# Kernel tuning notes

Measured on AMD Instinct MI355X. Metric: run time of the kernel, lower is better.

## Reference

```python
import jax, jax.numpy as jnp
import numpy as np

N = 50000       # nodes
E = 800000      # edges (avg degree 16)
IN = 256        # input feature dim
HID = 64        # per-head hidden dim
H = 2           # heads
C = 64          # num_classes (final single-head layer width)
NEG_SLOPE = 0.01  # torch F.leaky_relu default


def setup_inputs() -> dict:
    key = jax.random.key(0)
    ks = jax.random.split(key, 24)
    nrm = lambda k, shape, scale: jax.random.normal(k, shape, jnp.float32) * scale
    features = nrm(ks[0], (N, IN), 1.0)
    src = jax.random.randint(ks[1], (E,), 0, N)
    dst = jax.random.randint(ks[2], (E,), 0, N)
    # layer 0: H heads, Linear(IN->HID) + attn_l/attn_r Linear(HID->1)
    W0 = nrm(ks[3], (H, IN, HID), IN ** -0.5)
    b0 = jnp.zeros((H, HID), jnp.float32)
    al0 = nrm(ks[4], (H, HID), HID ** -0.5)
    bl0 = jnp.zeros((H,), jnp.float32)
    ar0 = nrm(ks[5], (H, HID), HID ** -0.5)
    br0 = jnp.zeros((H,), jnp.float32)
    # layer 1: H heads, Linear(H*HID->HID)
    W1 = nrm(ks[6], (H, H * HID, HID), (H * HID) ** -0.5)
    b1 = jnp.zeros((H, HID), jnp.float32)
    al1 = nrm(ks[7], (H, HID), HID ** -0.5)
    bl1 = jnp.zeros((H,), jnp.float32)
    ar1 = nrm(ks[8], (H, HID), HID ** -0.5)
    br1 = jnp.zeros((H,), jnp.float32)
    # final: 1 head, Linear(H*HID->C)
    Wf = nrm(ks[9], (1, H * HID, C), (H * HID) ** -0.5)
    bf = jnp.zeros((1, C), jnp.float32)
    alf = nrm(ks[10], (1, C), C ** -0.5)
    blf = jnp.zeros((1,), jnp.float32)
    arf = nrm(ks[11], (1, C), C ** -0.5)
    brf = jnp.zeros((1,), jnp.float32)
    return dict(features=features, src=src, dst=dst,
                W0=W0, b0=b0, al0=al0, bl0=bl0, ar0=ar0, br0=br0,
                W1=W1, b1=b1, al1=al1, bl1=bl1, ar1=ar1, br1=br1,
                Wf=Wf, bf=bf, alf=alf, blf=blf, arf=arf, brf=brf)


def gat_layer(x, src, dst, W, b, al, bl, ar, br):
    # x: [N, D]; W: [H, D, K]
    ft = jnp.einsum('nd,hdk->nhk', x, W) + b          # [N,H,K]
    a1 = jnp.einsum('nhk,hk->nh', ft, al) + bl        # [N,H] (dst-side)
    a2 = jnp.einsum('nhk,hk->nh', ft, ar) + br        # [N,H] (src-side)
    s = jax.nn.leaky_relu(a1[dst] + a2[src], NEG_SLOPE)  # [E,H]
    m = jax.ops.segment_max(s, dst, num_segments=N)      # per-dst max for stable softmax
    e = jnp.exp(s - m[dst])
    denom = jax.ops.segment_sum(e, dst, num_segments=N)
    alpha = e / denom[dst]                               # edge softmax over in-neighbors
    accum = jax.ops.segment_sum(alpha[:, :, None] * ft[src], dst, num_segments=N)  # [N,H,K]
    return jax.nn.elu(accum)


def reference(features, src, dst,
              W0, b0, al0, bl0, ar0, br0,
              W1, b1, al1, bl1, ar1, br1,
              Wf, bf, alf, blf, arf, brf):
    x = gat_layer(features, src, dst, W0, b0, al0, bl0, ar0, br0).reshape(N, H * HID)
    x = gat_layer(x, src, dst, W1, b1, al1, bl1, ar1, br1).reshape(N, H * HID)
    out = gat_layer(x, src, dst, Wf, bf, alf, blf, arf, brf)[:, 0, :]  # [N,C]
    return out
```

## Files before the change

kernel.cpp:

```cpp
#include <hip/hip_runtime.h>
#include <math.h>

#define NN 50000
#define EE 800000
#define DIN 256
#define NEG_SLOPE 0.01f

typedef __attribute__((ext_vector_type(8))) short bf16x8;
typedef __attribute__((ext_vector_type(8))) unsigned short u16x8;
typedef __attribute__((ext_vector_type(4))) float f32x4;
typedef __attribute__((ext_vector_type(2))) _Float16 f16x2;

__device__ __forceinline__ unsigned short bf16_rne(float f) {
    unsigned int u = __float_as_uint(f);
    u += 0x7fffu + ((u >> 16) & 1u);
    return (unsigned short)(u >> 16);
}
__device__ __forceinline__ float bf16_tof(unsigned short h) {
    return __uint_as_float(((unsigned int)h) << 16);
}

__device__ __forceinline__ void fmamix_lo(float& a, unsigned f, float w) {
    asm("v_fma_mix_f32 %0, %1, %2, %0 op_sel:[0,0,0] op_sel_hi:[1,0,0]"
        : "+v"(a)
        : "v"(f), "v"(w));
}
__device__ __forceinline__ void fmamix_hi(float& a, unsigned f, float w) {
    asm("v_fma_mix_f32 %0, %1, %2, %0 op_sel:[1,0,0] op_sel_hi:[1,0,0]"
        : "+v"(a)
        : "v"(f), "v"(w));
}

__global__ __launch_bounds__(1024) void scanA_kernel(const int* __restrict__ cnt,
                                                     int* __restrict__ off,
                                                     int* __restrict__ aux, int Nn) {
    __shared__ int wsums[16];
    int tid = threadIdx.x, lane = tid & 63, w = tid >> 6;
    int i = blockIdx.x * 1024 + tid;
    int v = (i < Nn) ? cnt[i] : 0;
    int x = v;
#pragma unroll
    for (int d = 1; d < 64; d <<= 1) {
        int y = __shfl_up(x, d);
        if (lane >= d) x += y;
    }
    if (lane == 63) wsums[w] = x;
    __syncthreads();
    if (w == 0 && lane < 16) {
        int ws = wsums[lane];
#pragma unroll
        for (int d = 1; d < 16; d <<= 1) {
            int y = __shfl_up(ws, d);
            if (lane >= d) ws += y;
        }
        wsums[lane] = ws;
    }
    __syncthreads();
    int incl = x + (w > 0 ? wsums[w - 1] : 0);
    if (i < Nn) off[i + 1] = incl;
    if (tid == 1023) aux[blockIdx.x] = incl;
}

__global__ __launch_bounds__(1024) void scanC_kernel(const int* __restrict__ aux,
                                                     int* __restrict__ off, int Nn) {
    int b = blockIdx.x;
    int prefix = 0;
    for (int j = 0; j < b; j++) prefix += aux[j];
    int i = b * 1024 + threadIdx.x;
    if (i < Nn) off[i + 1] += prefix;
    if (i == 0 && b == 0) off[0] = 0;
}

__global__ __launch_bounds__(256) void scatter_kernel(const int* __restrict__ src,
                                                      const int* __restrict__ dst,
                                                      const int* __restrict__ off,
                                                      const int* __restrict__ pos,
                                                      int* __restrict__ esrc, int E) {
    int e = blockIdx.x * 256 + threadIdx.x;
    if (e >= E) return;
    int d = dst[e];
    esrc[off[d] + pos[e]] = src[e];
}

__global__ __launch_bounds__(256) void conv_w_kernel(
    const float* __restrict__ W0, const float* __restrict__ W1,
    const float* __restrict__ Wf, unsigned short* __restrict__ w0h,
    unsigned short* __restrict__ w0l, unsigned short* __restrict__ w1h,
    unsigned short* __restrict__ w1l, unsigned short* __restrict__ wfh,
    unsigned short* __restrict__ wfl) {
    int t = blockIdx.x * 256 + threadIdx.x;
    const float* W;
    unsigned short *oh, *ol;
    int D, u;
    if (t < 32768) { W = W0; oh = w0h; ol = w0l; D = 256; u = t; }
    else if (t < 49152) { W = W1; oh = w1h; ol = w1l; D = 128; u = t - 32768; }
    else if (t < 57344) { W = Wf; oh = wfh; ol = wfl; D = 128; u = t - 49152; }
    else return;
    int d = u & (D - 1);
    int n = u / D;
    float v = W[((size_t)(n >> 6) * D + d) * 64 + (n & 63)];
    unsigned short hi = bf16_rne(v);
    unsigned short lo = bf16_rne(v - bf16_tof(hi));
    oh[(size_t)n * D + d] = hi;
    ol[(size_t)n * D + d] = lo;
}

#define LDK 40

template <int NCOL, bool AFP32, bool HIST>
__global__ __launch_bounds__(256) void gemm_attn(
    const float* __restrict__ Xf, const unsigned short* __restrict__ Xhi,
    const unsigned short* __restrict__ Xlo, const unsigned short* __restrict__ Wthi,
    const unsigned short* __restrict__ Wtlo, const float* __restrict__ bias,
    const float* __restrict__ al, const float* __restrict__ bl,
    const float* __restrict__ ar, const float* __restrict__ br,
    _Float16* __restrict__ FT, float* __restrict__ A1, float* __restrict__ A2,
    int Nn, int D, const int* __restrict__ edst, int* __restrict__ cnt,
    int* __restrict__ pos, int E, int gemmBlocks) {
    if (HIST) {
        if ((int)blockIdx.x >= gemmBlocks) {
            int e = ((int)blockIdx.x - gemmBlocks) * 256 + threadIdx.x;
            if (e < E) pos[e] = atomicAdd(&cnt[edst[e]], 1);
            return;
        }
    }
    const int H = NCOL / 64;
    const int NC16 = NCOL / 16;
    __shared__ __align__(16) unsigned short Ahi_s[64 * LDK];
    __shared__ __align__(16) unsigned short Alo_s[64 * LDK];
    __shared__ __align__(16) unsigned short Bhi_s[NCOL * LDK];
    __shared__ __align__(16) unsigned short Blo_s[NCOL * LDK];

    int tid = threadIdx.x;
    int wv = tid >> 6, l = tid & 63, lm = l & 15, quad = l >> 4;
    int m0 = blockIdx.x * 64;

    f32x4 acc[NC16];
#pragma unroll
    for (int c = 0; c < NC16; c++) acc[c] = (f32x4){0.f, 0.f, 0.f, 0.f};

    for (int d0 = 0; d0 < D; d0 += 32) {
        if (AFP32) {
#pragma unroll
            for (int i = 0; i < 2; i++) {
                int u = tid + i * 256;
                int row = u >> 3, c4 = u & 7;
                float4 v = make_float4(0.f, 0.f, 0.f, 0.f);
                if (m0 + row < Nn)
                    v = *(const float4*)&Xf[(size_t)(m0 + row) * D + d0 + c4 * 4];
                float f[4] = {v.x, v.y, v.z, v.w};
                unsigned short hi[4], lo[4];
#pragma unroll
                for (int j = 0; j < 4; j++) {
                    hi[j] = bf16_rne(f[j]);
                    lo[j] = bf16_rne(f[j] - bf16_tof(hi[j]));
                }
                *(ushort4*)&Ahi_s[row * LDK + c4 * 4] = make_ushort4(hi[0], hi[1], hi[2], hi[3]);
                *(ushort4*)&Alo_s[row * LDK + c4 * 4] = make_ushort4(lo[0], lo[1], lo[2], lo[3]);
            }
        } else {
            int row = tid >> 2, q = tid & 3;
            u16x8 vh = (u16x8)0, vl = (u16x8)0;
            if (m0 + row < Nn) {
                vh = *(const u16x8*)&Xhi[(size_t)(m0 + row) * D + d0 + q * 8];
                vl = *(const u16x8*)&Xlo[(size_t)(m0 + row) * D + d0 + q * 8];
            }
            *(u16x8*)&Ahi_s[row * LDK + q * 8] = vh;
            *(u16x8*)&Alo_s[row * LDK + q * 8] = vl;
        }
#pragma unroll
        for (int i = 0; i < NCOL / 64; i++) {
            int u = tid + i * 256;
            int n = u >> 2, q = u & 3;
            *(u16x8*)&Bhi_s[n * LDK + q * 8] =
                *(const u16x8*)&Wthi[(size_t)n * D + d0 + q * 8];
            *(u16x8*)&Blo_s[n * LDK + q * 8] =
                *(const u16x8*)&Wtlo[(size_t)n * D + d0 + q * 8];
        }
        __syncthreads();

        int arow = wv * 16 + lm;
        bf16x8 ah = *(const bf16x8*)&Ahi_s[arow * LDK + quad * 8];
        bf16x8 alo = *(const bf16x8*)&Alo_s[arow * LDK + quad * 8];
#pragma unroll
        for (int cg = 0; cg < NC16; cg += 4) {
            bf16x8 bh4[4], bl4[4];
#pragma unroll
            for (int u = 0; u < 4; u++) {
                bh4[u] = *(const bf16x8*)&Bhi_s[((cg + u) * 16 + lm) * LDK + quad * 8];
                bl4[u] = *(const bf16x8*)&Blo_s[((cg + u) * 16 + lm) * LDK + quad * 8];
            }
#pragma unroll
            for (int u = 0; u < 4; u++)
                acc[cg + u] = __builtin_amdgcn_mfma_f32_16x16x32_bf16(ah, bh4[u], acc[cg + u], 0, 0, 0);
#pragma unroll
            for (int u = 0; u < 4; u++)
                acc[cg + u] = __builtin_amdgcn_mfma_f32_16x16x32_bf16(ah, bl4[u], acc[cg + u], 0, 0, 0);
#pragma unroll
            for (int u = 0; u < 4; u++)
                acc[cg + u] = __builtin_amdgcn_mfma_f32_16x16x32_bf16(alo, bh4[u], acc[cg + u], 0, 0, 0);
        }
        __syncthreads();
    }

    float bj[NC16], alj[NC16], arj[NC16];
#pragma unroll
    for (int c = 0; c < NC16; c++) {
        bj[c] = bias[c * 16 + lm];
        alj[c] = al[c * 16 + lm];
        arj[c] = ar[c * 16 + lm];
    }
#pragma unroll
    for (int reg = 0; reg < 4; reg++) {
        int row = m0 + wv * 16 + quad * 4 + reg;
        bool ok = row < Nn;
        float s1[H], s2[H];
#pragma unroll
        for (int h = 0; h < H; h++) { s1[h] = 0.f; s2[h] = 0.f; }
#pragma unroll
        for (int c = 0; c < NC16; c++) {
            float o = acc[c][reg] + bj[c];
            int h = c >> 2;
            s1[h] += o * alj[c];
            s2[h] += o * arj[c];
            if (ok) FT[(size_t)row * NCOL + c * 16 + lm] = (_Float16)o;
        }
#pragma unroll
        for (int h = 0; h < H; h++) {
#pragma unroll
            for (int d = 1; d < 16; d <<= 1) {
                s1[h] += __shfl_xor(s1[h], d);
                s2[h] += __shfl_xor(s2[h], d);
            }
        }
        if (ok && lm == 0) {
#pragma unroll
            for (int h = 0; h < H; h++) {
                A1[(size_t)row * H + h] = s1[h] + bl[h];
                A2[(size_t)row * H + h] = s2[h] + br[h];
            }
        }
    }
}

__global__ __launch_bounds__(256) void agg2_kernel(
    const _Float16* __restrict__ ft, const float* __restrict__ a1,
    const float* __restrict__ a2, const int* __restrict__ off,
    const int* __restrict__ esrc, unsigned short* __restrict__ ohi,
    unsigned short* __restrict__ olo, int Nn) {
    __shared__ __align__(16) int2 pk0s[4][64];
    __shared__ __align__(16) int2 pk1s[4][64];
    int wv = threadIdx.x >> 6, lane = threadIdx.x & 63;
    int n = blockIdx.x * 4 + wv;
    if (n >= Nn) return;
    int o0 = off[n], deg = off[n + 1] - o0;
    int hs = lane >> 5, cl2 = lane * 2;
    unsigned lb = (unsigned)lane * 4u;
    if (deg == 0) {
        *(ushort2*)&ohi[(size_t)n * 128 + cl2] = make_ushort2(0, 0);
        *(ushort2*)&olo[(size_t)n * 128 + cl2] = make_ushort2(0, 0);
        return;
    }
    const char* ftb = (const char*)ft;
    const int2* pw = hs ? pk1s[wv] : pk0s[wv];
    float2 a1v = *(const float2*)&a1[(size_t)n * 2];
    float ax = 0.f, ay = 0.f;
    float ds0 = 0.f, ds1 = 0.f;
    for (int e0 = 0; e0 < deg; e0 += 64) {
        int nE = min(64, deg - e0);
        float w0 = 0.f, w1 = 0.f;
        int sj = 0;
        if (lane < nE) {
            sj = esrc[o0 + e0 + lane];
            float2 a2j = *(const float2*)((const char*)a2 + ((unsigned)sj << 3));
            float t0 = a1v.x + a2j.x;
            float t1 = a1v.y + a2j.y;
            t0 = t0 > 0.f ? t0 : NEG_SLOPE * t0;
            t1 = t1 > 0.f ? t1 : NEG_SLOPE * t1;
            w0 = __expf(t0);
            w1 = __expf(t1);
        }
        ds0 += w0;
        ds1 += w1;
        pk0s[wv][lane] = make_int2(sj, __float_as_int(w0));
        pk1s[wv][lane] = make_int2(sj, __float_as_int(w1));
        int nB = (nE + 15) >> 4;
        for (int b = 0; b < nB; b++) {
            int j = b * 16;
            int2 pb[16];
#pragma unroll
            for (int u = 0; u < 16; u++) pb[u] = pw[j + u];
            unsigned f[16];
#pragma unroll
            for (int u = 0; u < 16; u++)
                f[u] = *(const unsigned*)(ftb + (((unsigned)pb[u].x << 8) + lb));
#pragma unroll
            for (int u = 0; u < 16; u++) {
                float w = __int_as_float(pb[u].y);
                fmamix_lo(ax, f[u], w);
                fmamix_hi(ay, f[u], w);
            }
        }
    }
#pragma unroll
    for (int d = 1; d < 64; d <<= 1) {
        ds0 += __shfl_xor(ds0, d);
        ds1 += __shfl_xor(ds1, d);
    }
    float rd = 1.f / (hs ? ds1 : ds0);
    float rx = ax * rd, ry = ay * rd;
    rx = rx > 0.f ? rx : expm1f(rx);
    ry = ry > 0.f ? ry : expm1f(ry);
    unsigned short hx = bf16_rne(rx), hy = bf16_rne(ry);
    unsigned short lx = bf16_rne(rx - bf16_tof(hx)), ly = bf16_rne(ry - bf16_tof(hy));
    *(ushort2*)&ohi[(size_t)n * 128 + cl2] = make_ushort2(hx, hy);
    *(ushort2*)&olo[(size_t)n * 128 + cl2] = make_ushort2(lx, ly);
}

__global__ __launch_bounds__(256) void agg1_kernel(
    const _Float16* __restrict__ ft, const float* __restrict__ a1,
    const float* __restrict__ a2, const int* __restrict__ off,
    const int* __restrict__ esrc, float* __restrict__ out, int Nn) {
    __shared__ __align__(16) int2 pks[4][64];
    int wv = threadIdx.x >> 6, lane = threadIdx.x & 63;
    int n = blockIdx.x * 4 + wv;
    if (n >= Nn) return;
    int o0 = off[n], deg = off[n + 1] - o0;
    if (deg == 0) {
        out[(size_t)n * 64 + lane] = 0.f;
        return;
    }
    const char* ftb = (const char*)ft;
    unsigned lb = (unsigned)lane * 2u;
    float a1v = a1[n];
    float acc = 0.f, dsum = 0.f;
    for (int e0 = 0; e0 < deg; e0 += 64) {
        int nE = min(64, deg - e0);
        float wl = 0.f;
        int sj = 0;
        if (lane < nE) {
            sj = esrc[o0 + e0 + lane];
            float t = a1v + a2[sj];
            t = t > 0.f ? t : NEG_SLOPE * t;
            wl = __expf(t);
        }
        dsum += wl;
        pks[wv][lane] = make_int2(sj, __float_as_int(wl));
        int nB = (nE + 15) >> 4;
        for (int b = 0; b < nB; b++) {
            int j = b * 16;
            int2 pb[16];
#pragma unroll
            for (int u = 0; u < 16; u++) pb[u] = pks[wv][j + u];
            unsigned f[16];
#pragma unroll
            for (int u = 0; u < 16; u++)
                f[u] = *(const unsigned short*)(ftb + (((unsigned)pb[u].x << 7) + lb));
#pragma unroll
            for (int u = 0; u < 16; u++)
                fmamix_lo(acc, f[u], __int_as_float(pb[u].y));
        }
    }
#pragma unroll
    for (int d = 1; d < 64; d <<= 1) dsum += __shfl_xor(dsum, d);
    float r = acc / dsum;
    out[(size_t)n * 64 + lane] = r > 0.f ? r : expm1f(r);
}

extern "C" void kernel_launch(void* const* d_in, const int* in_sizes, int n_in,
                              void* d_out, int out_size, void* d_ws, size_t ws_size,
                              hipStream_t stream) {
    const float* features = (const float*)d_in[0];
    const int* src = (const int*)d_in[1];
    const int* dst = (const int*)d_in[2];
    const float* W0 = (const float*)d_in[3];
    const float* b0 = (const float*)d_in[4];
    const float* al0 = (const float*)d_in[5];
    const float* bl0 = (const float*)d_in[6];
    const float* ar0 = (const float*)d_in[7];
    const float* br0 = (const float*)d_in[8];
    const float* W1 = (const float*)d_in[9];
    const float* b1 = (const float*)d_in[10];
    const float* al1 = (const float*)d_in[11];
    const float* bl1 = (const float*)d_in[12];
    const float* ar1 = (const float*)d_in[13];
    const float* br1 = (const float*)d_in[14];
    const float* Wf = (const float*)d_in[15];
    const float* bf = (const float*)d_in[16];
    const float* alf = (const float*)d_in[17];
    const float* blf = (const float*)d_in[18];
    const float* arf = (const float*)d_in[19];
    const float* brf = (const float*)d_in[20];

    char* p = (char*)d_ws;
    auto carve = [&](size_t bytes) {
        void* q = (void*)p;
        p += (bytes + 255) & ~(size_t)255;
        return q;
    };
    _Float16* ft = (_Float16*)carve((size_t)NN * 128 * 2);
    unsigned short* Xhi = (unsigned short*)carve((size_t)NN * 128 * 2);
    unsigned short* Xlo = (unsigned short*)carve((size_t)NN * 128 * 2);
    float* a1 = (float*)carve((size_t)NN * 2 * 4);
    float* a2 = (float*)carve((size_t)NN * 2 * 4);
    int* off = (int*)carve((size_t)(NN + 1) * 4);
    int* cnt = (int*)carve((size_t)NN * 4);
    int* esrc = (int*)carve((size_t)EE * 4);
    int* pos = (int*)carve((size_t)EE * 4);
    int* aux = (int*)carve(64 * 4);
    unsigned short* w0h = (unsigned short*)carve(32768 * 2);
    unsigned short* w0l = (unsigned short*)carve(32768 * 2);
    unsigned short* w1h = (unsigned short*)carve(16384 * 2);
    unsigned short* w1l = (unsigned short*)carve(16384 * 2);
    unsigned short* wfh = (unsigned short*)carve(8192 * 2);
    unsigned short* wfl = (unsigned short*)carve(8192 * 2);

    const int NB_SCAN = (NN + 1023) / 1024;
    const int GE = (EE + 255) / 256;

    const int gx = (NN + 63) / 64;
    const int gn = (NN + 3) / 4;

    hipMemsetAsync(cnt, 0, (size_t)NN * 4, stream);
    conv_w_kernel<<<(57344 + 255) / 256, 256, 0, stream>>>(W0, W1, Wf, w0h, w0l, w1h,
                                                           w1l, wfh, wfl);

    gemm_attn<128, true, true><<<gx + GE, 256, 0, stream>>>(
        features, nullptr, nullptr, w0h, w0l, b0, al0, bl0, ar0, br0, ft, a1, a2,
        NN, DIN, dst, cnt, pos, EE, gx);

    scanA_kernel<<<NB_SCAN, 1024, 0, stream>>>(cnt, off, aux, NN);
    scanC_kernel<<<NB_SCAN, 1024, 0, stream>>>(aux, off, NN);
    scatter_kernel<<<GE, 256, 0, stream>>>(src, dst, off, pos, esrc, EE);

    agg2_kernel<<<gn, 256, 0, stream>>>(ft, a1, a2, off, esrc, Xhi, Xlo, NN);

    gemm_attn<128, false, false><<<gx, 256, 0, stream>>>(
        nullptr, Xhi, Xlo, w1h, w1l, b1, al1, bl1, ar1, br1, ft, a1, a2, NN, 128,
        nullptr, nullptr, nullptr, 0, 0);
    agg2_kernel<<<gn, 256, 0, stream>>>(ft, a1, a2, off, esrc, Xhi, Xlo, NN);

    gemm_attn<64, false, false><<<gx, 256, 0, stream>>>(
        nullptr, Xhi, Xlo, wfh, wfl, bf, alf, blf, arf, brf, ft, a1, a2, NN, 128,
        nullptr, nullptr, nullptr, 0, 0);
    agg1_kernel<<<gn, 256, 0, stream>>>(ft, a1, a2, off, esrc, (float*)d_out, NN);
}
```

Before: 301.6 us.

## Double GEMM row tile to 128 so each wave reuses B fragments across two row groups

The fused GEMM+attention kernel now computes 128 rows per block instead of 64. Each wave handles two 16-row groups with separate accumulators, so every B-fragment load from shared memory feeds twice as many MFMAs and the weight tile is staged half as often overall. The cost is double the accumulator registers and a larger LDS footprint, which may lower occupancy. The grid also halves, to about 391 GEMM blocks, which cuts parallelism on a many-CU GPU.

```diff
diff --git a/kernel.cpp b/kernel.cpp
--- a/kernel.cpp
+++ b/kernel.cpp
@@ -9,7 +9,6 @@
 typedef __attribute__((ext_vector_type(8))) short bf16x8;
 typedef __attribute__((ext_vector_type(8))) unsigned short u16x8;
 typedef __attribute__((ext_vector_type(4))) float f32x4;
-typedef __attribute__((ext_vector_type(2))) _Float16 f16x2;
 
 __device__ __forceinline__ unsigned short bf16_rne(float f) {
     unsigned int u = __float_as_uint(f);
@@ -126,23 +125,25 @@
     }
     const int H = NCOL / 64;
     const int NC16 = NCOL / 16;
-    __shared__ __align__(16) unsigned short Ahi_s[64 * LDK];
-    __shared__ __align__(16) unsigned short Alo_s[64 * LDK];
+    __shared__ __align__(16) unsigned short Ahi_s[128 * LDK];
+    __shared__ __align__(16) unsigned short Alo_s[128 * LDK];
     __shared__ __align__(16) unsigned short Bhi_s[NCOL * LDK];
     __shared__ __align__(16) unsigned short Blo_s[NCOL * LDK];
 
     int tid = threadIdx.x;
     int wv = tid >> 6, l = tid & 63, lm = l & 15, quad = l >> 4;
-    int m0 = blockIdx.x * 64;
-
-    f32x4 acc[NC16];
-#pragma unroll
-    for (int c = 0; c < NC16; c++) acc[c] = (f32x4){0.f, 0.f, 0.f, 0.f};
+    int m0 = blockIdx.x * 128;
+
+    f32x4 acc[2][NC16];
+#pragma unroll
+    for (int rg = 0; rg < 2; rg++)
+#pragma unroll
+        for (int c = 0; c < NC16; c++) acc[rg][c] = (f32x4){0.f, 0.f, 0.f, 0.f};
 
     for (int d0 = 0; d0 < D; d0 += 32) {
         if (AFP32) {
 #pragma unroll
-            for (int i = 0; i < 2; i++) {
+            for (int i = 0; i < 4; i++) {
                 int u = tid + i * 256;
                 int row = u >> 3, c4 = u & 7;
                 float4 v = make_float4(0.f, 0.f, 0.f, 0.f);
@@ -159,14 +160,18 @@
                 *(ushort4*)&Alo_s[row * LDK + c4 * 4] = make_ushort4(lo[0], lo[1], lo[2], lo[3]);
             }
         } else {
-            int row = tid >> 2, q = tid & 3;
-            u16x8 vh = (u16x8)0, vl = (u16x8)0;
-            if (m0 + row < Nn) {
-                vh = *(const u16x8*)&Xhi[(size_t)(m0 + row) * D + d0 + q * 8];
-                vl = *(const u16x8*)&Xlo[(size_t)(m0 + row) * D + d0 + q * 8];
-            }
-            *(u16x8*)&Ahi_s[row * LDK + q * 8] = vh;
-            *(u16x8*)&Alo_s[row * LDK + q * 8] = vl;
+#pragma unroll
+            for (int i = 0; i < 2; i++) {
+                int u = tid + i * 256;
+                int row = u >> 2, q = u & 3;
+                u16x8 vh = (u16x8)0, vl = (u16x8)0;
+                if (m0 + row < Nn) {
+                    vh = *(const u16x8*)&Xhi[(size_t)(m0 + row) * D + d0 + q * 8];
+                    vl = *(const u16x8*)&Xlo[(size_t)(m0 + row) * D + d0 + q * 8];
+                }
+                *(u16x8*)&Ahi_s[row * LDK + q * 8] = vh;
+                *(u16x8*)&Alo_s[row * LDK + q * 8] = vl;
+            }
         }
 #pragma unroll
         for (int i = 0; i < NCOL / 64; i++) {
@@ -179,9 +184,11 @@
         }
         __syncthreads();
 
-        int arow = wv * 16 + lm;
-        bf16x8 ah = *(const bf16x8*)&Ahi_s[arow * LDK + quad * 8];
-        bf16x8 alo = *(const bf16x8*)&Alo_s[arow * LDK + quad * 8];
+        int arow = wv * 32 + lm;
+        bf16x8 ah0 = *(const bf16x8*)&Ahi_s[arow * LDK + quad * 8];
+        bf16x8 al0 = *(const bf16x8*)&Alo_s[arow * LDK + quad * 8];
+        bf16x8 ah1 = *(const bf16x8*)&Ahi_s[(arow + 16) * LDK + quad * 8];
+        bf16x8 al1 = *(const bf16x8*)&Alo_s[(arow + 16) * LDK + quad * 8];
 #pragma unroll
         for (int cg = 0; cg < NC16; cg += 4) {
             bf16x8 bh4[4], bl4[4];
@@ -192,13 +199,22 @@
             }
 #pragma unroll
             for (int u = 0; u < 4; u++)
-                acc[cg + u] = __builtin_amdgcn_mfma_f32_16x16x32_bf16(ah, bh4[u], acc[cg + u], 0, 0, 0);
-#pragma unroll
-            for (int u = 0; u < 4; u++)
-                acc[cg + u] = __builtin_amdgcn_mfma_f32_16x16x32_bf16(ah, bl4[u], acc[cg + u], 0, 0, 0);
-#pragma unroll
-            for (int u = 0; u < 4; u++)
-                acc[cg + u] = __builtin_amdgcn_mfma_f32_16x16x32_bf16(alo, bh4[u], acc[cg + u], 0, 0, 0);
+                acc[0][cg + u] = __builtin_amdgcn_mfma_f32_16x16x32_bf16(ah0, bh4[u], acc[0][cg + u], 0, 0, 0);
+#pragma unroll
+            for (int u = 0; u < 4; u++)
+                acc[1][cg + u] = __builtin_amdgcn_mfma_f32_16x16x32_bf16(ah1, bh4[u], acc[1][cg + u], 0, 0, 0);
+#pragma unroll
+            for (int u = 0; u < 4; u++)
+                acc[0][cg + u] = __builtin_amdgcn_mfma_f32_16x16x32_bf16(ah0, bl4[u], acc[0][cg + u], 0, 0, 0);
+#pragma unroll
+            for (int u = 0; u < 4; u++)
+                acc[1][cg + u] = __builtin_amdgcn_mfma_f32_16x16x32_bf16(ah1, bl4[u], acc[1][cg + u], 0, 0, 0);
+#pragma unroll
+            for (int u = 0; u < 4; u++)
+                acc[0][cg + u] = __builtin_amdgcn_mfma_f32_16x16x32_bf16(al0, bh4[u], acc[0][cg + u], 0, 0, 0);
+#pragma unroll
+            for (int u = 0; u < 4; u++)
+                acc[1][cg + u] = __builtin_amdgcn_mfma_f32_16x16x32_bf16(al1, bh4[u], acc[1][cg + u], 0, 0, 0);
         }
         __syncthreads();
     }
@@ -211,33 +227,36 @@
         arj[c] = ar[c * 16 + lm];
     }
 #pragma unroll
-    for (int reg = 0; reg < 4; reg++) {
-        int row = m0 + wv * 16 + quad * 4 + reg;
-        bool ok = row < Nn;
-        float s1[H], s2[H];
-#pragma unroll
-        for (int h = 0; h < H; h++) { s1[h] = 0.f; s2[h] = 0.f; }
-#pragma unroll
-        for (int c = 0; c < NC16; c++) {
-            float o = acc[c][reg] + bj[c];
-            int h = c >> 2;
-            s1[h] += o * alj[c];
-            s2[h] += o * arj[c];
-            if (ok) FT[(size_t)row * NCOL + c * 16 + lm] = (_Float16)o;
-        }
-#pragma unroll
-        for (int h = 0; h < H; h++) {
-#pragma unroll
-            for (int d = 1; d < 16; d <<= 1) {
-                s1[h] += __shfl_xor(s1[h], d);
-                s2[h] += __shfl_xor(s2[h], d);
-            }
-        }
-        if (ok && lm == 0) {
+    for (int rg = 0; rg < 2; rg++) {
+#pragma unroll
+        for (int reg = 0; reg < 4; reg++) {
+            int row = m0 + wv * 32 + rg * 16 + quad * 4 + reg;
+            bool ok = row < Nn;
+            float s1[H], s2[H];
+#pragma unroll
+            for (int h = 0; h < H; h++) { s1[h] = 0.f; s2[h] = 0.f; }
+#pragma unroll
+            for (int c = 0; c < NC16; c++) {
+                float o = acc[rg][c][reg] + bj[c];
+                int h = c >> 2;
+                s1[h] += o * alj[c];
+                s2[h] += o * arj[c];
+                if (ok) FT[(size_t)row * NCOL + c * 16 + lm] = (_Float16)o;
+            }
 #pragma unroll
             for (int h = 0; h < H; h++) {
-                A1[(size_t)row * H + h] = s1[h] + bl[h];
-                A2[(size_t)row * H + h] = s2[h] + br[h];
+#pragma unroll
+                for (int d = 1; d < 16; d <<= 1) {
+                    s1[h] += __shfl_xor(s1[h], d);
+                    s2[h] += __shfl_xor(s2[h], d);
+                }
+            }
+            if (ok && lm == 0) {
+#pragma unroll
+                for (int h = 0; h < H; h++) {
+                    A1[(size_t)row * H + h] = s1[h] + bl[h];
+                    A2[(size_t)row * H + h] = s2[h] + br[h];
+                }
             }
         }
     }
@@ -418,7 +437,7 @@
     const int NB_SCAN = (NN + 1023) / 1024;
     const int GE = (EE + 255) / 256;
 
-    const int gx = (NN + 63) / 64;
+    const int gx = (NN + 127) / 128;
     const int gn = (NN + 3) / 4;
 
     hipMemsetAsync(cnt, 0, (size_t)NN * 4, stream);
```

Result: slower. 322.8 us (+7.0%).

## Bucket CSR edges by source range to improve gather locality

Applied to the files above, without the earlier changes.

The CSR build now uses a composite key of destination and source high bits (8 buckets of 8192 sources), so each node's in-edges are grouped by source region. The intent is to make the feature gathers in the aggregation kernels hit nearby memory in the cache in turn. The cost is an 8x larger count/offset array: a bigger memset, a scan with about 391 blocks whose scanC loops serially over prior block sums, and more histogram atomics spread over more keys.

```diff
diff --git a/kernel.cpp b/kernel.cpp
--- a/kernel.cpp
+++ b/kernel.cpp
@@ -5,11 +5,13 @@
 #define EE 800000
 #define DIN 256
 #define NEG_SLOPE 0.01f
+#define RB 8
+#define RSH 13
+#define NKEY (NN * RB)
 
 typedef __attribute__((ext_vector_type(8))) short bf16x8;
 typedef __attribute__((ext_vector_type(8))) unsigned short u16x8;
 typedef __attribute__((ext_vector_type(4))) float f32x4;
-typedef __attribute__((ext_vector_type(2))) _Float16 f16x2;
 
 __device__ __forceinline__ unsigned short bf16_rne(float f) {
     unsigned int u = __float_as_uint(f);
@@ -33,11 +35,11 @@
 
 __global__ __launch_bounds__(1024) void scanA_kernel(const int* __restrict__ cnt,
                                                      int* __restrict__ off,
-                                                     int* __restrict__ aux, int Nn) {
+                                                     int* __restrict__ aux, int Nb) {
     __shared__ int wsums[16];
     int tid = threadIdx.x, lane = tid & 63, w = tid >> 6;
     int i = blockIdx.x * 1024 + tid;
-    int v = (i < Nn) ? cnt[i] : 0;
+    int v = (i < Nb) ? cnt[i] : 0;
     int x = v;
 #pragma unroll
     for (int d = 1; d < 64; d <<= 1) {
@@ -57,29 +59,30 @@
     }
     __syncthreads();
     int incl = x + (w > 0 ? wsums[w - 1] : 0);
-    if (i < Nn) off[i + 1] = incl;
+    if (i < Nb) off[i + 1] = incl;
     if (tid == 1023) aux[blockIdx.x] = incl;
 }
 
 __global__ __launch_bounds__(1024) void scanC_kernel(const int* __restrict__ aux,
-                                                     int* __restrict__ off, int Nn) {
+                                                     int* __restrict__ off, int Nb) {
     int b = blockIdx.x;
     int prefix = 0;
     for (int j = 0; j < b; j++) prefix += aux[j];
     int i = b * 1024 + threadIdx.x;
-    if (i < Nn) off[i + 1] += prefix;
+    if (i < Nb) off[i + 1] += prefix;
     if (i == 0 && b == 0) off[0] = 0;
 }
 
 __global__ __launch_bounds__(256) void scatter_kernel(const int* __restrict__ src,
                                                       const int* __restrict__ dst,
-                                                      const int* __restrict__ off,
+                                                      const int* __restrict__ koff,
                                                       const int* __restrict__ pos,
                                                       int* __restrict__ esrc, int E) {
     int e = blockIdx.x * 256 + threadIdx.x;
     if (e >= E) return;
-    int d = dst[e];
-    esrc[off[d] + pos[e]] = src[e];
+    int s = src[e];
+    int key = dst[e] * RB + (s >> RSH);
+    esrc[koff[key] + pos[e]] = s;
 }
 
 __global__ __launch_bounds__(256) void conv_w_kernel(
@@ -115,12 +118,15 @@
     const float* __restrict__ al, const float* __restrict__ bl,
     const float* __restrict__ ar, const float* __restrict__ br,
     _Float16* __restrict__ FT, float* __restrict__ A1, float* __restrict__ A2,
-    int Nn, int D, const int* __restrict__ edst, int* __restrict__ cnt,
-    int* __restrict__ pos, int E, int gemmBlocks) {
+    int Nn, int D, const int* __restrict__ esrcin, const int* __restrict__ edst,
+    int* __restrict__ cnt, int* __restrict__ pos, int E, int gemmBlocks) {
     if (HIST) {
         if ((int)blockIdx.x >= gemmBlocks) {
             int e = ((int)blockIdx.x - gemmBlocks) * 256 + threadIdx.x;
-            if (e < E) pos[e] = atomicAdd(&cnt[edst[e]], 1);
+            if (e < E) {
+                int key = edst[e] * RB + (esrcin[e] >> RSH);
+                pos[e] = atomicAdd(&cnt[key], 1);
+            }
             return;
         }
     }
@@ -245,7 +251,7 @@
 
 __global__ __launch_bounds__(256) void agg2_kernel(
     const _Float16* __restrict__ ft, const float* __restrict__ a1,
-    const float* __restrict__ a2, const int* __restrict__ off,
+    const float* __restrict__ a2, const int* __restrict__ koff,
     const int* __restrict__ esrc, unsigned short* __restrict__ ohi,
     unsigned short* __restrict__ olo, int Nn) {
     __shared__ __align__(16) int2 pk0s[4][64];
@@ -253,7 +259,7 @@
     int wv = threadIdx.x >> 6, lane = threadIdx.x & 63;
     int n = blockIdx.x * 4 + wv;
     if (n >= Nn) return;
-    int o0 = off[n], deg = off[n + 1] - o0;
+    int o0 = koff[n * RB], deg = koff[n * RB + RB] - o0;
     int hs = lane >> 5, cl2 = lane * 2;
     unsigned lb = (unsigned)lane * 4u;
     if (deg == 0) {
@@ -319,13 +325,13 @@
 
 __global__ __launch_bounds__(256) void agg1_kernel(
     const _Float16* __restrict__ ft, const float* __restrict__ a1,
-    const float* __restrict__ a2, const int* __restrict__ off,
+    const float* __restrict__ a2, const int* __restrict__ koff,
     const int* __restrict__ esrc, float* __restrict__ out, int Nn) {
     __shared__ __align__(16) int2 pks[4][64];
     int wv = threadIdx.x >> 6, lane = threadIdx.x & 63;
     int n = blockIdx.x * 4 + wv;
     if (n >= Nn) return;
-    int o0 = off[n], deg = off[n + 1] - o0;
+    int o0 = koff[n * RB], deg = koff[n * RB + RB] - o0;
     if (deg == 0) {
         out[(size_t)n * 64 + lane] = 0.f;
         return;
@@ -403,11 +409,11 @@
     unsigned short* Xlo = (unsigned short*)carve((size_t)NN * 128 * 2);
     float* a1 = (float*)carve((size_t)NN * 2 * 4);
     float* a2 = (float*)carve((size_t)NN * 2 * 4);
-    int* off = (int*)carve((size_t)(NN + 1) * 4);
-    int* cnt = (int*)carve((size_t)NN * 4);
+    int* koff = (int*)carve((size_t)(NKEY + 1) * 4);
+    int* cnt = (int*)carve((size_t)NKEY * 4);
     int* esrc = (int*)carve((size_t)EE * 4);
     int* pos = (int*)carve((size_t)EE * 4);
-    int* aux = (int*)carve(64 * 4);
+    int* aux = (int*)carve(512 * 4);
     unsigned short* w0h = (unsigned short*)carve(32768 * 2);
     unsigned short* w0l = (unsigned short*)carve(32768 * 2);
     unsigned short* w1h = (unsigned short*)carve(16384 * 2);
@@ -415,33 +421,33 @@
     unsigned short* wfh = (unsigned short*)carve(8192 * 2);
     unsigned short* wfl = (unsigned short*)carve(8192 * 2);
 
-    const int NB_SCAN = (NN + 1023) / 1024;
+    const int NB_SCAN = (NKEY + 1023) / 1024;
     const int GE = (EE + 255) / 256;
 
     const int gx = (NN + 63) / 64;
     const int gn = (NN + 3) / 4;
 
-    hipMemsetAsync(cnt, 0, (size_t)NN * 4, stream);
+    hipMemsetAsync(cnt, 0, (size_t)NKEY * 4, stream);
     conv_w_kernel<<<(57344 + 255) / 256, 256, 0, stream>>>(W0, W1, Wf, w0h, w0l, w1h,
                                                            w1l, wfh, wfl);
 
     gemm_attn<128, true, true><<<gx + GE, 256, 0, stream>>>(
         features, nullptr, nullptr, w0h, w0l, b0, al0, bl0, ar0, br0, ft, a1, a2,
-        NN, DIN, dst, cnt, pos, EE, gx);
-
-    scanA_kernel<<<NB_SCAN, 1024, 0, stream>>>(cnt, off, aux, NN);
-    scanC_kernel<<<NB_SCAN, 1024, 0, stream>>>(aux, off, NN);
-    scatter_kernel<<<GE, 256, 0, stream>>>(src, dst, off, pos, esrc, EE);
-
-    agg2_kernel<<<gn, 256, 0, stream>>>(ft, a1, a2, off, esrc, Xhi, Xlo, NN);
+        NN, DIN, src, dst, cnt, pos, EE, gx);
+
+    scanA_kernel<<<NB_SCAN, 1024, 0, stream>>>(cnt, koff, aux, NKEY);
+    scanC_kernel<<<NB_SCAN, 1024, 0, stream>>>(aux, koff, NKEY);
+    scatter_kernel<<<GE, 256, 0, stream>>>(src, dst, koff, pos, esrc, EE);
+
+    agg2_kernel<<<gn, 256, 0, stream>>>(ft, a1, a2, koff, esrc, Xhi, Xlo, NN);
 
     gemm_attn<128, false, false><<<gx, 256, 0, stream>>>(
         nullptr, Xhi, Xlo, w1h, w1l, b1, al1, bl1, ar1, br1, ft, a1, a2, NN, 128,
-        nullptr, nullptr, nullptr, 0, 0);
-    agg2_kernel<<<gn, 256, 0, stream>>>(ft, a1, a2, off, esrc, Xhi, Xlo, NN);
+        nullptr, nullptr, nullptr, nullptr, 0, 0);
+    agg2_kernel<<<gn, 256, 0, stream>>>(ft, a1, a2, koff, esrc, Xhi, Xlo, NN);
 
     gemm_attn<64, false, false><<<gx, 256, 0, stream>>>(
         nullptr, Xhi, Xlo, wfh, wfl, bf, alf, blf, arf, brf, ft, a1, a2, NN, 128,
-        nullptr, nullptr, nullptr, 0, 0);
-    agg1_kernel<<<gn, 256, 0, stream>>>(ft, a1, a2, off, esrc, (float*)d_out, NN);
-}
+        nullptr, nullptr, nullptr, nullptr, 0, 0);
+    agg1_kernel<<<gn, 256, 0, stream>>>(ft, a1, a2, koff, esrc, (float*)d_out, NN);
+}
```

Measured after the change: 315.8 us. 4.7% more time.
